# Performance work log

Measured on AMD Instinct MI355X. Metric: run time of the kernel, lower is better.

## Reference

```python
import jax, jax.numpy as jnp
import numpy as np

K = 16  # neighbors per node (knn_graph, loop=False)


def setup_inputs() -> dict:
    key = jax.random.key(0)
    ks = jax.random.split(key, 4)
    B, N = 32, 2048
    coords = jax.random.normal(ks[0], (B, N, 3), jnp.float32)

    def lin(k, i, o):  # glorot-ish init
        return jax.random.normal(k, (i, o), jnp.float32) / np.sqrt(i).astype(np.float32)

    return {
        "coords": coords,
        "W1": lin(ks[1], 3, 64),   "b1": jnp.zeros((64,), jnp.float32),
        "W2": lin(ks[2], 64, 128), "b2": jnp.zeros((128,), jnp.float32),
        "Wf": lin(ks[3], 128, 128), "bf": jnp.zeros((128,), jnp.float32),
    }


def _knn_idx(c, k):
    # c: [N,3] -> [N,k] indices of k nearest neighbors (self excluded, loop=False)
    n = c.shape[0]
    d2 = jnp.sum((c[:, None, :] - c[None, :, :]) ** 2, axis=-1)  # [N,N]
    d2 = jnp.where(jnp.eye(n, dtype=bool), jnp.inf, d2)
    _, idx = jax.lax.top_k(-d2, k)  # smallest distances
    return idx


def _gcn(x, nbr_self, W, b):
    # PyG GCNConv with add_self_loops: every node has in-degree exactly k+1
    # (k knn edges + self-loop), so the symmetric gcn_norm
    # 1/sqrt(deg_i*deg_j) reduces to the constant 1/(k+1).
    h = x @ W                                   # [N,out]
    agg = h[nbr_self].sum(axis=1) / nbr_self.shape[1]
    return agg + b


def reference(coords, W1, b1, W2, b2, Wf, bf):
    n = coords.shape[1]

    def per_sample(c):
        nbr = _knn_idx(c, K)                                     # [N,K]
        nbr_self = jnp.concatenate([nbr, jnp.arange(n)[:, None]], axis=1)  # [N,K+1]
        x = jax.nn.relu(_gcn(c, nbr_self, W1, b1))
        x = jax.nn.relu(_gcn(x, nbr_self, W2, b2))
        return x @ Wf + bf                                       # [N,128]

    return jax.vmap(per_sample)(coords)  # [B,N,128]
```

## Files before the change

kernel.cpp:

```cpp
#include <hip/hip_runtime.h>
#include <hip/hip_bf16.h>

typedef unsigned int u32;
typedef __attribute__((ext_vector_type(8))) short bf16x8;
typedef __attribute__((ext_vector_type(4))) float f32x4;

#define N_NODES 2048
#define INF __builtin_inff()

__device__ __forceinline__ float bflo(u32 u){ return __uint_as_float(u << 16); }
__device__ __forceinline__ float bfhi(u32 u){ return __uint_as_float(u & 0xFFFF0000u); }
__device__ __forceinline__ u32 packbf(float a, float b){
  u32 ua = __float_as_uint(a), ub = __float_as_uint(b);
  u32 ra = (ua + 0x7FFFu + ((ua >> 16) & 1u)) >> 16;
  u32 rb = (ub + 0x7FFFu + ((ub >> 16) & 1u)) >> 16;
  return ra | (rb << 16);
}

__device__ __forceinline__ float dist2(float cx, float cy, float cz,
                                       float jx, float jy, float jz) {
  float dx = cx - jx, dy = cy - jy, dz = cz - jz;
  return fmaf(dz, dz, fmaf(dy, dy, dx * dx));
}

__device__ __forceinline__ float mkk(float d, int j) {
  return __uint_as_float((__float_as_uint(d) & 0xFFFFF800u) | (u32)j);
}

__device__ __forceinline__ void ins8(float (&ad)[8], float v) {
#pragma unroll
  for (int t = 7; t >= 1; --t)
    ad[t] = __builtin_amdgcn_fmed3f(v, ad[t-1], ad[t]);
  ad[0] = fminf(ad[0], v);
}
__device__ __forceinline__ void ins16(float (&ad)[16], float v) {
#pragma unroll
  for (int t = 15; t >= 1; --t)
    ad[t] = __builtin_amdgcn_fmed3f(v, ad[t-1], ad[t]);
  ad[0] = fminf(ad[0], v);
}

__device__ __forceinline__ void merge8s(float (&ad)[16], int tid) {
#define CED(I, J) { float lo_ = fminf(ad[I], ad[J]); ad[J] = fmaxf(ad[I], ad[J]); ad[I] = lo_; }
#define CLEAN16 \
  CED(0,8) CED(1,9) CED(2,10) CED(3,11) CED(4,12) CED(5,13) CED(6,14) CED(7,15) \
  CED(0,4) CED(1,5) CED(2,6)  CED(3,7)  CED(8,12) CED(9,13) CED(10,14) CED(11,15) \
  CED(0,2) CED(1,3) CED(4,6)  CED(5,7)  CED(8,10) CED(9,11) CED(12,14) CED(13,15) \
  CED(0,1) CED(2,3) CED(4,5)  CED(6,7)  CED(8,9)  CED(10,11) CED(12,13) CED(14,15)
  float bd[16];
#pragma unroll
  for (int q = 0; q < 16; ++q) bd[q] = __shfl(ad[q], tid ^ 1);
#pragma unroll
  for (int q = 0; q < 16; ++q) ad[q] = fminf(ad[q], bd[15 - q]);
  CLEAN16
#pragma unroll
  for (int q = 0; q < 16; ++q) bd[q] = __shfl(ad[q], tid ^ 2);
#pragma unroll
  for (int q = 0; q < 16; ++q) ad[q] = fminf(ad[q], bd[15 - q]);
  CLEAN16
#pragma unroll
  for (int q = 0; q < 16; ++q) bd[q] = __shfl(ad[q], tid ^ 4);
#pragma unroll
  for (int q = 0; q < 16; ++q) ad[q] = fminf(ad[q], bd[15 - q]);
  CLEAN16
#undef CLEAN16
#undef CED
}

__device__ __forceinline__ bool node_try8(
    const float (&ad)[8], int tid, int sub, int& j0, int& j1)
{
  const float myMax = ad[7];
  float md[16];
#pragma unroll
  for (int q = 0; q < 8; ++q) md[q] = ad[q];
#pragma unroll
  for (int q = 8; q < 16; ++q) md[q] = __uint_as_float(0x7F000000u);
  merge8s(md, tid);
  const float md15 = md[15];
  float mnext = INF;
#pragma unroll
  for (int q = 7; q >= 0; --q) mnext = (ad[q] > md15) ? ad[q] : mnext;
  float c17 = fminf(mnext, __shfl(mnext, tid ^ 1));
  c17 = fminf(c17, __shfl(c17, tid ^ 2));
  c17 = fminf(c17, __shfl(c17, tid ^ 4));
  float mnext2 = INF;
#pragma unroll
  for (int q = 7; q >= 0; --q) mnext2 = (ad[q] > c17) ? ad[q] : mnext2;
  float c18 = fminf(mnext2, __shfl(mnext2, tid ^ 1));
  c18 = fminf(c18, __shfl(c18, tid ^ 2));
  c18 = fminf(c18, __shfl(c18, tid ^ 4));
  const u32 t17 = __float_as_uint(c17) & 0xFFFFF800u;
  const u32 t18 = __float_as_uint(c18) & 0xFFFFF800u;
  md[0] = c17;
  j0 = (int)(__float_as_uint(md[(sub<<1)+0]) & 0x7FFu);
  j1 = (int)(__float_as_uint(md[(sub<<1)+1]) & 0x7FFu);
  return (myMax >= c18) && (t18 >= t17 + 0x800u);
}

__device__ __forceinline__ void node_fb8(
    int node, int tid, int sub, int ln,
    float cx, float cy, float cz, const float* cs,
    u32 (*nbuf)[16], u32* ncnt, int& j0, int& j1)
{
  float a3[16];
#pragma unroll
  for (int q = 0; q < 16; ++q) a3[q] = INF;
#pragma unroll 1
  for (int it = 0; it < 64; ++it) {
    const int v4 = (it << 3) + sub;
    const float4* p = (const float4*)(cs + v4 * 12);
    float4 p0 = p[0], p1 = p[1], p2 = p[2];
    const int base = v4 << 2;
    float d0 = (base + 0 == node) ? INF : dist2(cx,cy,cz, p0.x,p0.y,p0.z);
    float d1 = (base + 1 == node) ? INF : dist2(cx,cy,cz, p0.w,p1.x,p1.y);
    float d2 = (base + 2 == node) ? INF : dist2(cx,cy,cz, p1.z,p1.w,p2.x);
    float d3 = (base + 3 == node) ? INF : dist2(cx,cy,cz, p2.y,p2.z,p2.w);
    ins16(a3, d0); ins16(a3, d1); ins16(a3, d2); ins16(a3, d3);
  }
  merge8s(a3, tid);
  const float tau = a3[15];
  if (sub == 0) ncnt[ln] = 0;
  __builtin_amdgcn_s_barrier();
#pragma unroll 1
  for (int it = 0; it < 64; ++it) {
    const int v4 = (it << 3) + sub;
    const float4* p = (const float4*)(cs + v4 * 12);
    float4 p0 = p[0], p1 = p[1], p2 = p[2];
    const int base = v4 << 2;
    float d0 = dist2(cx,cy,cz, p0.x,p0.y,p0.z);
    float d1 = dist2(cx,cy,cz, p0.w,p1.x,p1.y);
    float d2 = dist2(cx,cy,cz, p1.z,p1.w,p2.x);
    float d3 = dist2(cx,cy,cz, p2.y,p2.z,p2.w);
    if (d0 <= tau && base + 0 != node) { u32 p_ = atomicAdd(&ncnt[ln], 1u); if (p_ < 16u) nbuf[ln][p_] = (u32)(base + 0); }
    if (d1 <= tau && base + 1 != node) { u32 p_ = atomicAdd(&ncnt[ln], 1u); if (p_ < 16u) nbuf[ln][p_] = (u32)(base + 1); }
    if (d2 <= tau && base + 2 != node) { u32 p_ = atomicAdd(&ncnt[ln], 1u); if (p_ < 16u) nbuf[ln][p_] = (u32)(base + 2); }
    if (d3 <= tau && base + 3 != node) { u32 p_ = atomicAdd(&ncnt[ln], 1u); if (p_ < 16u) nbuf[ln][p_] = (u32)(base + 3); }
  }
  __builtin_amdgcn_s_barrier();
  j0 = (int)nbuf[ln][(sub << 1) + 0];
  j1 = (int)nbuf[ln][(sub << 1) + 1];
}

__global__ __launch_bounds__(256) void k1_knn_l1(
    const float* __restrict__ coords, const float* __restrict__ W1,
    const float* __restrict__ b1, int* __restrict__ nbr, u32* __restrict__ x1)
{
  __shared__ float ldsc[N_NODES * 3];
  __shared__ u32   nbuf[32][16];
  __shared__ u32   ncnt[32];
  __shared__ float w1s[192];
  __shared__ float b1s[64];
  const int tid   = threadIdx.x;
  const int s     = blockIdx.x >> 6;
  const int chunk = blockIdx.x & 63;
  const float* cg = coords + (size_t)s * (N_NODES * 3);
  {
    const float4* src = (const float4*)cg;
    float4* dst = (float4*)ldsc;
#pragma unroll
    for (int q = 0; q < 6; ++q) dst[tid + (q << 8)] = src[tid + (q << 8)];
  }
  if (tid < 192) w1s[tid] = W1[tid];
  if (tid < 64)  b1s[tid] = b1[tid];
  __syncthreads();

  const int ln   = tid >> 3;
  const int sub  = tid & 7;
  const int node = (chunk << 5) + ln;
  const float cx = ldsc[3*node], cy = ldsc[3*node+1], cz = ldsc[3*node+2];

  float ad[8];
#pragma unroll
  for (int q = 0; q < 8; ++q) ad[q] = INF;

#define LOAD6(P0,P1,P2,P3,P4,P5, ITV) {                                   \
    const int v4a_ = ((ITV) << 4) + sub;                                  \
    const float4* pa_ = (const float4*)(ldsc + v4a_ * 12);                \
    const float4* pb_ = (const float4*)(ldsc + (v4a_ + 8) * 12);          \
    P0 = pa_[0]; P1 = pa_[1]; P2 = pa_[2];                                \
    P3 = pb_[0]; P4 = pb_[1]; P5 = pb_[2]; }

#define BODY(P0,P1,P2,P3,P4,P5, ITV) {                                    \
    const int ba_ = (((ITV) << 4) + sub) << 2, bb_ = ba_ + 32;            \
    ins8(ad, mkk(dist2(cx,cy,cz, P0.x,P0.y,P0.z),   ba_+0));              \
    ins8(ad, mkk(dist2(cx,cy,cz, P0.w,P1.x,P1.y),   ba_+1));              \
    ins8(ad, mkk(dist2(cx,cy,cz, P1.z,P1.w,P2.x),   ba_+2));              \
    ins8(ad, mkk(dist2(cx,cy,cz, P2.y,P2.z,P2.w),   ba_+3));              \
    ins8(ad, mkk(dist2(cx,cy,cz, P3.x,P3.y,P3.z),   bb_+0));              \
    ins8(ad, mkk(dist2(cx,cy,cz, P3.w,P4.x,P4.y),   bb_+1));              \
    ins8(ad, mkk(dist2(cx,cy,cz, P4.z,P4.w,P5.x),   bb_+2));              \
    ins8(ad, mkk(dist2(cx,cy,cz, P5.y,P5.z,P5.w),   bb_+3)); }

  {
    float4 A0, A1, A2, A3, A4, A5, B0, B1, B2, B3, B4, B5;
    LOAD6(A0,A1,A2,A3,A4,A5, 0)
#pragma unroll 1
    for (int it = 0; it < 32; it += 2) {
      LOAD6(B0,B1,B2,B3,B4,B5, it + 1)
      BODY (A0,A1,A2,A3,A4,A5, it)
      LOAD6(A0,A1,A2,A3,A4,A5, (it + 2) & 31)
      BODY (B0,B1,B2,B3,B4,B5, it + 1)
    }
  }
#undef LOAD6
#undef BODY

  int j0, j1;
  const bool ok = node_try8(ad, tid, sub, j0, j1);
  if (!__all((int)ok)) {
    node_fb8(node, tid, sub, ln, cx, cy, cz, ldsc, nbuf, ncnt, j0, j1);
  }

  const size_t gnode = ((size_t)s << 11) + node;
  *(int2*)(nbr + gnode * 16 + (sub << 1)) = make_int2(j0, j1);

  float sx, sy, sz;
  if (sub == 0) { sx = cx; sy = cy; sz = cz; } else { sx = 0.f; sy = 0.f; sz = 0.f; }
  sx += ldsc[3*j0]   + ldsc[3*j1];
  sy += ldsc[3*j0+1] + ldsc[3*j1+1];
  sz += ldsc[3*j0+2] + ldsc[3*j1+2];
  sx += __shfl_xor(sx, 1); sx += __shfl_xor(sx, 2); sx += __shfl_xor(sx, 4);
  sy += __shfl_xor(sy, 1); sy += __shfl_xor(sy, 2); sy += __shfl_xor(sy, 4);
  sz += __shfl_xor(sz, 1); sz += __shfl_xor(sz, 2); sz += __shfl_xor(sz, 4);
  const float inv = 1.0f / 17.0f;
  float mx = sx * inv, my = sy * inv, mz = sz * inv;

  u32 pk[4];
#pragma unroll
  for (int oo = 0; oo < 8; oo += 2) {
    const int o = (sub << 3) + oo;
    float v0 = fmaf(mz, w1s[128+o],   fmaf(my, w1s[64+o],   fmaf(mx, w1s[o],   b1s[o])));
    float v1 = fmaf(mz, w1s[128+o+1], fmaf(my, w1s[64+o+1], fmaf(mx, w1s[o+1], b1s[o+1])));
    pk[oo >> 1] = packbf(fmaxf(v0, 0.0f), fmaxf(v1, 0.0f));
  }
  *(uint4*)(x1 + gnode * 32 + (sub << 2)) = make_uint4(pk[0], pk[1], pk[2], pk[3]);
}

__global__ __launch_bounds__(256) void k2_gcn2(
    const u32* __restrict__ x1, const int* __restrict__ nbr,
    const float* __restrict__ W2, const float* __restrict__ b2,
    u32* __restrict__ x2)
{
  __shared__ uint4 AldsV[1024];
  __shared__ uint4 BhiV[1024];
  __shared__ uint4 BloV[1024];
  char* Alds = (char*)AldsV; char* Bhi = (char*)BhiV; char* Blo = (char*)BloV;
  const int tid   = threadIdx.x;
  const int node0 = blockIdx.x << 7;

#pragma unroll
  for (int i = 0; i < 32; ++i) {
    int e = tid + (i << 8);
    int k = e >> 7, n = e & 127;
    float w = W2[e];
    u32 hb = packbf(w, 0.0f) & 0xFFFFu;
    float whi = __uint_as_float(hb << 16);
    u32 lb = packbf(w - whi, 0.0f) & 0xFFFFu;
    int byte = n * 128 + ((2 * k) ^ ((n & 7) << 4));
    *(unsigned short*)(Bhi + byte) = (unsigned short)hb;
    *(unsigned short*)(Blo + byte) = (unsigned short)lb;
  }

  {
    const int r = tid >> 1, half = tid & 1;
    const size_t gnode = (size_t)node0 + r;
    const u32* selfp = x1 + gnode * 32 + half * 16;
    const u32* x1s   = x1 + ((gnode >> 11) << 11) * 32;
    const int* nb    = nbr + gnode * 16;
    float a[32];
#pragma unroll
    for (int q = 0; q < 4; ++q) {
      uint4 v = *(const uint4*)(selfp + (q << 2));
      a[8*q+0] = bflo(v.x); a[8*q+1] = bfhi(v.x);
      a[8*q+2] = bflo(v.y); a[8*q+3] = bfhi(v.y);
      a[8*q+4] = bflo(v.z); a[8*q+5] = bfhi(v.z);
      a[8*q+6] = bflo(v.w); a[8*q+7] = bfhi(v.w);
    }
#pragma unroll
    for (int t = 0; t < 16; ++t) {
      const u32* rp = x1s + (size_t)nb[t] * 32 + half * 16;
#pragma unroll
      for (int q = 0; q < 4; ++q) {
        uint4 v = *(const uint4*)(rp + (q << 2));
        a[8*q+0] += bflo(v.x); a[8*q+1] += bfhi(v.x);
        a[8*q+2] += bflo(v.y); a[8*q+3] += bfhi(v.y);
        a[8*q+4] += bflo(v.z); a[8*q+5] += bfhi(v.z);
        a[8*q+6] += bflo(v.w); a[8*q+7] += bfhi(v.w);
      }
    }
    const float inv = 1.0f / 17.0f;
    u32 pk[16];
#pragma unroll
    for (int j = 0; j < 16; ++j)
      pk[j] = packbf(a[2*j] * inv, a[2*j+1] * inv);
#pragma unroll
    for (int q = 0; q < 4; ++q) {
      int byte = r * 128 + ((((half << 6) + (q << 4))) ^ ((r & 7) << 4));
      *(uint4*)(Alds + byte) = make_uint4(pk[4*q], pk[4*q+1], pk[4*q+2], pk[4*q+3]);
    }
  }
  __syncthreads();

  const int lane = tid & 63, wv = tid >> 6;
  const int cl = lane & 15, kg = lane >> 4;

  f32x4 acc[2][8];
#pragma unroll
  for (int rt = 0; rt < 2; ++rt)
#pragma unroll
    for (int ct = 0; ct < 8; ++ct) {
      float bv = b2[(ct << 4) + cl];
      acc[rt][ct] = (f32x4){bv, bv, bv, bv};
    }

#pragma unroll
  for (int ks = 0; ks < 2; ++ks) {
    const int kb = (ks << 6) + (kg << 4);
    bf16x8 af[2];
#pragma unroll
    for (int rt = 0; rt < 2; ++rt) {
      int row = (wv << 5) + (rt << 4) + cl;
      af[rt] = *(const bf16x8*)(Alds + row * 128 + (kb ^ ((row & 7) << 4)));
    }
#pragma unroll
    for (int ct = 0; ct < 8; ++ct) {
      int n = (ct << 4) + cl;
      int byte = n * 128 + (kb ^ ((n & 7) << 4));
      bf16x8 bh = *(const bf16x8*)(Bhi + byte);
      bf16x8 bl = *(const bf16x8*)(Blo + byte);
#pragma unroll
      for (int rt = 0; rt < 2; ++rt) {
        acc[rt][ct] = __builtin_amdgcn_mfma_f32_16x16x32_bf16(af[rt], bh, acc[rt][ct], 0, 0, 0);
        acc[rt][ct] = __builtin_amdgcn_mfma_f32_16x16x32_bf16(af[rt], bl, acc[rt][ct], 0, 0, 0);
      }
    }
  }

  unsigned short* x2h = (unsigned short*)x2;
#pragma unroll
  for (int rt = 0; rt < 2; ++rt)
#pragma unroll
    for (int ct = 0; ct < 8; ++ct) {
      int colg = (ct << 4) + cl;
      int nr0  = node0 + (wv << 5) + (rt << 4) + (kg << 2);
#pragma unroll
      for (int r = 0; r < 4; ++r) {
        float v = fmaxf(acc[rt][ct][r], 0.0f);
        x2h[(size_t)(nr0 + r) * 128 + colg] = (unsigned short)(packbf(v, 0.0f) & 0xFFFFu);
      }
    }
}

__global__ __launch_bounds__(256) void k3_final(
    const u32* __restrict__ x2, const float* __restrict__ Wf,
    const float* __restrict__ bfv, float* __restrict__ out)
{
  __shared__ uint4 AldsV[2048];
  __shared__ uint4 BhiV[1024];
  __shared__ uint4 BloV[1024];
  char* Alds = (char*)AldsV; char* Bhi = (char*)BhiV; char* Blo = (char*)BloV;
  const int tid   = threadIdx.x;
  const int node0 = (blockIdx.x >> 1) << 7;
  const int ch0   = (blockIdx.x & 1) << 6;

#pragma unroll
  for (int i = 0; i < 32; ++i) {
    int e = tid + (i << 8);
    int k = e >> 6, n = e & 63;
    float w = Wf[k * 128 + ch0 + n];
    u32 hb = packbf(w, 0.0f) & 0xFFFFu;
    float whi = __uint_as_float(hb << 16);
    u32 lb = packbf(w - whi, 0.0f) & 0xFFFFu;
    int byte = n * 256 + ((2 * k) ^ ((n & 15) << 4));
    *(unsigned short*)(Bhi + byte) = (unsigned short)hb;
    *(unsigned short*)(Blo + byte) = (unsigned short)lb;
  }

  {
    const int r = tid >> 1, half = tid & 1;
    const u32* src = x2 + (size_t)(node0 + r) * 64 + half * 32;
#pragma unroll
    for (int q = 0; q < 8; ++q) {
      uint4 v = *(const uint4*)(src + (q << 2));
      int byte = r * 256 + ((((half << 7) + (q << 4))) ^ ((r & 15) << 4));
      *(uint4*)(Alds + byte) = v;
    }
  }
  __syncthreads();

  const int lane = tid & 63, wv = tid >> 6;
  const int cl = lane & 15, kg = lane >> 4;

  f32x4 acc[2][4];
#pragma unroll
  for (int rt = 0; rt < 2; ++rt)
#pragma unroll
    for (int ct = 0; ct < 4; ++ct) {
      float bv = bfv[ch0 + (ct << 4) + cl];
      acc[rt][ct] = (f32x4){bv, bv, bv, bv};
    }

#pragma unroll
  for (int ks = 0; ks < 4; ++ks) {
    const int kb = (ks << 6) + (kg << 4);
    bf16x8 af[2];
#pragma unroll
    for (int rt = 0; rt < 2; ++rt) {
      int row = (wv << 5) + (rt << 4) + cl;
      af[rt] = *(const bf16x8*)(Alds + row * 256 + (kb ^ ((row & 15) << 4)));
    }
#pragma unroll
    for (int ct = 0; ct < 4; ++ct) {
      int n = (ct << 4) + cl;
      int byte = n * 256 + (kb ^ ((n & 15) << 4));
      bf16x8 bh = *(const bf16x8*)(Bhi + byte);
      bf16x8 bl = *(const bf16x8*)(Blo + byte);
#pragma unroll
      for (int rt = 0; rt < 2; ++rt) {
        acc[rt][ct] = __builtin_amdgcn_mfma_f32_16x16x32_bf16(af[rt], bh, acc[rt][ct], 0, 0, 0);
        acc[rt][ct] = __builtin_amdgcn_mfma_f32_16x16x32_bf16(af[rt], bl, acc[rt][ct], 0, 0, 0);
      }
    }
  }

#pragma unroll
  for (int rt = 0; rt < 2; ++rt)
#pragma unroll
    for (int ct = 0; ct < 4; ++ct) {
      int col = ch0 + (ct << 4) + cl;
      int nr0 = node0 + (wv << 5) + (rt << 4) + (kg << 2);
#pragma unroll
      for (int r = 0; r < 4; ++r)
        out[(size_t)(nr0 + r) * 128 + col] = acc[rt][ct][r];
    }
}

extern "C" void kernel_launch(void* const* d_in, const int* in_sizes, int n_in,
                              void* d_out, int out_size, void* d_ws, size_t ws_size,
                              hipStream_t stream) {
  const float* coords = (const float*)d_in[0];
  const float* W1 = (const float*)d_in[1];
  const float* b1 = (const float*)d_in[2];
  const float* W2 = (const float*)d_in[3];
  const float* b2 = (const float*)d_in[4];
  const float* Wf = (const float*)d_in[5];
  const float* bf = (const float*)d_in[6];
  float* out = (float*)d_out;

  char* ws = (char*)d_ws;
  int* nbr = (int*)ws;
  u32* x1  = (u32*)(ws + (size_t)4  * 1024 * 1024);
  u32* x2  = (u32*)(ws + (size_t)12 * 1024 * 1024);

  k1_knn_l1<<<2048, 256, 0, stream>>>(coords, W1, b1, nbr, x1);
  k2_gcn2  <<< 512, 256, 0, stream>>>(x1, nbr, W2, b2, x2);
  k3_final <<<1024, 256, 0, stream>>>(x2, Wf, bf, out);
}
```

Baseline: 160.0 us.

## Process two query nodes per lane group in kNN kernel to reuse coordinate loads

Each 8-lane group now computes the kNN scans for two nodes at once. Every candidate coordinate loaded from LDS is reused for two distance evaluations, halving LDS traffic per distance and the number of blocks. The fallback path now synchronises with an lgkmcnt wait instead of a workgroup barrier, since each slot is owned by a single 8-lane group. The cost is doubled register use for the two sorted lists, which can lower occupancy, and fewer blocks (1024) to fill the GPU.

```diff
diff --git a/kernel.cpp b/kernel.cpp
--- a/kernel.cpp
+++ b/kernel.cpp
@@ -99,7 +99,7 @@
 }
 
 __device__ __forceinline__ void node_fb8(
-    int node, int tid, int sub, int ln,
+    int node, int tid, int sub, int slot,
     float cx, float cy, float cz, const float* cs,
     u32 (*nbuf)[16], u32* ncnt, int& j0, int& j1)
 {
@@ -120,8 +120,8 @@
   }
   merge8s(a3, tid);
   const float tau = a3[15];
-  if (sub == 0) ncnt[ln] = 0;
-  __builtin_amdgcn_s_barrier();
+  if (sub == 0) ncnt[slot] = 0;
+  asm volatile("s_waitcnt lgkmcnt(0)" ::: "memory");
 #pragma unroll 1
   for (int it = 0; it < 64; ++it) {
     const int v4 = (it << 3) + sub;
@@ -132,14 +132,14 @@
     float d1 = dist2(cx,cy,cz, p0.w,p1.x,p1.y);
     float d2 = dist2(cx,cy,cz, p1.z,p1.w,p2.x);
     float d3 = dist2(cx,cy,cz, p2.y,p2.z,p2.w);
-    if (d0 <= tau && base + 0 != node) { u32 p_ = atomicAdd(&ncnt[ln], 1u); if (p_ < 16u) nbuf[ln][p_] = (u32)(base + 0); }
-    if (d1 <= tau && base + 1 != node) { u32 p_ = atomicAdd(&ncnt[ln], 1u); if (p_ < 16u) nbuf[ln][p_] = (u32)(base + 1); }
-    if (d2 <= tau && base + 2 != node) { u32 p_ = atomicAdd(&ncnt[ln], 1u); if (p_ < 16u) nbuf[ln][p_] = (u32)(base + 2); }
-    if (d3 <= tau && base + 3 != node) { u32 p_ = atomicAdd(&ncnt[ln], 1u); if (p_ < 16u) nbuf[ln][p_] = (u32)(base + 3); }
-  }
-  __builtin_amdgcn_s_barrier();
-  j0 = (int)nbuf[ln][(sub << 1) + 0];
-  j1 = (int)nbuf[ln][(sub << 1) + 1];
+    if (d0 <= tau && base + 0 != node) { u32 p_ = atomicAdd(&ncnt[slot], 1u); if (p_ < 16u) nbuf[slot][p_] = (u32)(base + 0); }
+    if (d1 <= tau && base + 1 != node) { u32 p_ = atomicAdd(&ncnt[slot], 1u); if (p_ < 16u) nbuf[slot][p_] = (u32)(base + 1); }
+    if (d2 <= tau && base + 2 != node) { u32 p_ = atomicAdd(&ncnt[slot], 1u); if (p_ < 16u) nbuf[slot][p_] = (u32)(base + 2); }
+    if (d3 <= tau && base + 3 != node) { u32 p_ = atomicAdd(&ncnt[slot], 1u); if (p_ < 16u) nbuf[slot][p_] = (u32)(base + 3); }
+  }
+  asm volatile("s_waitcnt lgkmcnt(0)" ::: "memory");
+  j0 = (int)nbuf[slot][(sub << 1) + 0];
+  j1 = (int)nbuf[slot][(sub << 1) + 1];
 }
 
 __global__ __launch_bounds__(256) void k1_knn_l1(
@@ -147,13 +147,13 @@
     const float* __restrict__ b1, int* __restrict__ nbr, u32* __restrict__ x1)
 {
   __shared__ float ldsc[N_NODES * 3];
-  __shared__ u32   nbuf[32][16];
-  __shared__ u32   ncnt[32];
+  __shared__ u32   nbuf[64][16];
+  __shared__ u32   ncnt[64];
   __shared__ float w1s[192];
   __shared__ float b1s[64];
   const int tid   = threadIdx.x;
-  const int s     = blockIdx.x >> 6;
-  const int chunk = blockIdx.x & 63;
+  const int s     = blockIdx.x >> 5;
+  const int chunk = blockIdx.x & 31;
   const float* cg = coords + (size_t)s * (N_NODES * 3);
   {
     const float4* src = (const float4*)cg;
@@ -165,14 +165,16 @@
   if (tid < 64)  b1s[tid] = b1[tid];
   __syncthreads();
 
-  const int ln   = tid >> 3;
-  const int sub  = tid & 7;
-  const int node = (chunk << 5) + ln;
-  const float cx = ldsc[3*node], cy = ldsc[3*node+1], cz = ldsc[3*node+2];
-
-  float ad[8];
-#pragma unroll
-  for (int q = 0; q < 8; ++q) ad[q] = INF;
+  const int ln    = tid >> 3;
+  const int sub   = tid & 7;
+  const int nodeA = (chunk << 6) + (ln << 1);
+  const int nodeB = nodeA + 1;
+  const float cxA = ldsc[3*nodeA], cyA = ldsc[3*nodeA+1], czA = ldsc[3*nodeA+2];
+  const float cxB = ldsc[3*nodeB], cyB = ldsc[3*nodeB+1], czB = ldsc[3*nodeB+2];
+
+  float adA[8], adB[8];
+#pragma unroll
+  for (int q = 0; q < 8; ++q) { adA[q] = INF; adB[q] = INF; }
 
 #define LOAD6(P0,P1,P2,P3,P4,P5, ITV) {                                   \
     const int v4a_ = ((ITV) << 4) + sub;                                  \
@@ -181,16 +183,22 @@
     P0 = pa_[0]; P1 = pa_[1]; P2 = pa_[2];                                \
     P3 = pb_[0]; P4 = pb_[1]; P5 = pb_[2]; }
 
+#define EVAL2(JX, JY, JZ, JIDX) {                                         \
+    float dA_ = dist2(cxA,cyA,czA, JX,JY,JZ);                             \
+    float dB_ = dist2(cxB,cyB,czB, JX,JY,JZ);                             \
+    ins8(adA, mkk(dA_, JIDX));                                            \
+    ins8(adB, mkk(dB_, JIDX)); }
+
 #define BODY(P0,P1,P2,P3,P4,P5, ITV) {                                    \
     const int ba_ = (((ITV) << 4) + sub) << 2, bb_ = ba_ + 32;            \
-    ins8(ad, mkk(dist2(cx,cy,cz, P0.x,P0.y,P0.z),   ba_+0));              \
-    ins8(ad, mkk(dist2(cx,cy,cz, P0.w,P1.x,P1.y),   ba_+1));              \
-    ins8(ad, mkk(dist2(cx,cy,cz, P1.z,P1.w,P2.x),   ba_+2));              \
-    ins8(ad, mkk(dist2(cx,cy,cz, P2.y,P2.z,P2.w),   ba_+3));              \
-    ins8(ad, mkk(dist2(cx,cy,cz, P3.x,P3.y,P3.z),   bb_+0));              \
-    ins8(ad, mkk(dist2(cx,cy,cz, P3.w,P4.x,P4.y),   bb_+1));              \
-    ins8(ad, mkk(dist2(cx,cy,cz, P4.z,P4.w,P5.x),   bb_+2));              \
-    ins8(ad, mkk(dist2(cx,cy,cz, P5.y,P5.z,P5.w),   bb_+3)); }
+    EVAL2(P0.x,P0.y,P0.z, ba_+0)                                          \
+    EVAL2(P0.w,P1.x,P1.y, ba_+1)                                          \
+    EVAL2(P1.z,P1.w,P2.x, ba_+2)                                          \
+    EVAL2(P2.y,P2.z,P2.w, ba_+3)                                          \
+    EVAL2(P3.x,P3.y,P3.z, bb_+0)                                          \
+    EVAL2(P3.w,P4.x,P4.y, bb_+1)                                          \
+    EVAL2(P4.z,P4.w,P5.x, bb_+2)                                          \
+    EVAL2(P5.y,P5.z,P5.w, bb_+3) }
 
   {
     float4 A0, A1, A2, A3, A4, A5, B0, B1, B2, B3, B4, B5;
@@ -204,37 +212,62 @@
     }
   }
 #undef LOAD6
+#undef EVAL2
 #undef BODY
 
-  int j0, j1;
-  const bool ok = node_try8(ad, tid, sub, j0, j1);
-  if (!__all((int)ok)) {
-    node_fb8(node, tid, sub, ln, cx, cy, cz, ldsc, nbuf, ncnt, j0, j1);
-  }
-
-  const size_t gnode = ((size_t)s << 11) + node;
-  *(int2*)(nbr + gnode * 16 + (sub << 1)) = make_int2(j0, j1);
-
-  float sx, sy, sz;
-  if (sub == 0) { sx = cx; sy = cy; sz = cz; } else { sx = 0.f; sy = 0.f; sz = 0.f; }
-  sx += ldsc[3*j0]   + ldsc[3*j1];
-  sy += ldsc[3*j0+1] + ldsc[3*j1+1];
-  sz += ldsc[3*j0+2] + ldsc[3*j1+2];
-  sx += __shfl_xor(sx, 1); sx += __shfl_xor(sx, 2); sx += __shfl_xor(sx, 4);
-  sy += __shfl_xor(sy, 1); sy += __shfl_xor(sy, 2); sy += __shfl_xor(sy, 4);
-  sz += __shfl_xor(sz, 1); sz += __shfl_xor(sz, 2); sz += __shfl_xor(sz, 4);
+  int jA0, jA1, jB0, jB1;
+  const bool okA = node_try8(adA, tid, sub, jA0, jA1);
+  const bool okB = node_try8(adB, tid, sub, jB0, jB1);
+  if (!__all((int)(okA && okB))) {
+    node_fb8(nodeA, tid, sub, (ln << 1) + 0, cxA, cyA, czA, ldsc, nbuf, ncnt, jA0, jA1);
+    node_fb8(nodeB, tid, sub, (ln << 1) + 1, cxB, cyB, czB, ldsc, nbuf, ncnt, jB0, jB1);
+  }
+
   const float inv = 1.0f / 17.0f;
-  float mx = sx * inv, my = sy * inv, mz = sz * inv;
-
-  u32 pk[4];
-#pragma unroll
-  for (int oo = 0; oo < 8; oo += 2) {
-    const int o = (sub << 3) + oo;
-    float v0 = fmaf(mz, w1s[128+o],   fmaf(my, w1s[64+o],   fmaf(mx, w1s[o],   b1s[o])));
-    float v1 = fmaf(mz, w1s[128+o+1], fmaf(my, w1s[64+o+1], fmaf(mx, w1s[o+1], b1s[o+1])));
-    pk[oo >> 1] = packbf(fmaxf(v0, 0.0f), fmaxf(v1, 0.0f));
-  }
-  *(uint4*)(x1 + gnode * 32 + (sub << 2)) = make_uint4(pk[0], pk[1], pk[2], pk[3]);
+  {
+    const size_t gnode = ((size_t)s << 11) + nodeA;
+    *(int2*)(nbr + gnode * 16 + (sub << 1)) = make_int2(jA0, jA1);
+    float sx, sy, sz;
+    if (sub == 0) { sx = cxA; sy = cyA; sz = czA; } else { sx = 0.f; sy = 0.f; sz = 0.f; }
+    sx += ldsc[3*jA0]   + ldsc[3*jA1];
+    sy += ldsc[3*jA0+1] + ldsc[3*jA1+1];
+    sz += ldsc[3*jA0+2] + ldsc[3*jA1+2];
+    sx += __shfl_xor(sx, 1); sx += __shfl_xor(sx, 2); sx += __shfl_xor(sx, 4);
+    sy += __shfl_xor(sy, 1); sy += __shfl_xor(sy, 2); sy += __shfl_xor(sy, 4);
+    sz += __shfl_xor(sz, 1); sz += __shfl_xor(sz, 2); sz += __shfl_xor(sz, 4);
+    float mx = sx * inv, my = sy * inv, mz = sz * inv;
+    u32 pk[4];
+#pragma unroll
+    for (int oo = 0; oo < 8; oo += 2) {
+      const int o = (sub << 3) + oo;
+      float v0 = fmaf(mz, w1s[128+o],   fmaf(my, w1s[64+o],   fmaf(mx, w1s[o],   b1s[o])));
+      float v1 = fmaf(mz, w1s[128+o+1], fmaf(my, w1s[64+o+1], fmaf(mx, w1s[o+1], b1s[o+1])));
+      pk[oo >> 1] = packbf(fmaxf(v0, 0.0f), fmaxf(v1, 0.0f));
+    }
+    *(uint4*)(x1 + gnode * 32 + (sub << 2)) = make_uint4(pk[0], pk[1], pk[2], pk[3]);
+  }
+  {
+    const size_t gnode = ((size_t)s << 11) + nodeB;
+    *(int2*)(nbr + gnode * 16 + (sub << 1)) = make_int2(jB0, jB1);
+    float sx, sy, sz;
+    if (sub == 0) { sx = cxB; sy = cyB; sz = czB; } else { sx = 0.f; sy = 0.f; sz = 0.f; }
+    sx += ldsc[3*jB0]   + ldsc[3*jB1];
+    sy += ldsc[3*jB0+1] + ldsc[3*jB1+1];
+    sz += ldsc[3*jB0+2] + ldsc[3*jB1+2];
+    sx += __shfl_xor(sx, 1); sx += __shfl_xor(sx, 2); sx += __shfl_xor(sx, 4);
+    sy += __shfl_xor(sy, 1); sy += __shfl_xor(sy, 2); sy += __shfl_xor(sy, 4);
+    sz += __shfl_xor(sz, 1); sz += __shfl_xor(sz, 2); sz += __shfl_xor(sz, 4);
+    float mx = sx * inv, my = sy * inv, mz = sz * inv;
+    u32 pk[4];
+#pragma unroll
+    for (int oo = 0; oo < 8; oo += 2) {
+      const int o = (sub << 3) + oo;
+      float v0 = fmaf(mz, w1s[128+o],   fmaf(my, w1s[64+o],   fmaf(mx, w1s[o],   b1s[o])));
+      float v1 = fmaf(mz, w1s[128+o+1], fmaf(my, w1s[64+o+1], fmaf(mx, w1s[o+1], b1s[o+1])));
+      pk[oo >> 1] = packbf(fmaxf(v0, 0.0f), fmaxf(v1, 0.0f));
+    }
+    *(uint4*)(x1 + gnode * 32 + (sub << 2)) = make_uint4(pk[0], pk[1], pk[2], pk[3]);
+  }
 }
 
 __global__ __launch_bounds__(256) void k2_gcn2(
@@ -453,7 +486,7 @@
   u32* x1  = (u32*)(ws + (size_t)4  * 1024 * 1024);
   u32* x2  = (u32*)(ws + (size_t)12 * 1024 * 1024);
 
-  k1_knn_l1<<<2048, 256, 0, stream>>>(coords, W1, b1, nbr, x1);
+  k1_knn_l1<<<1024, 256, 0, stream>>>(coords, W1, b1, nbr, x1);
   k2_gcn2  <<< 512, 256, 0, stream>>>(x1, nbr, W2, b2, x2);
   k3_final <<<1024, 256, 0, stream>>>(x2, Wf, bf, out);
 }
```

Result: slower. 185.9 us (+16.2%).
